# Kernel optimization log

Hardware: AMD Instinct MI355X
Metric: run time of the kernel (lower is better)

The kernel has to match this reference:

```python
import jax, jax.numpy as jnp
import numpy as np

DIM = 512
HEADS = 8
HEAD_DIM = DIM // HEADS
B, N = 2, 16 * 14 * 14  # input_size=(16,14,14) -> N=3136
SCALE = HEAD_DIM ** -0.5


def setup_inputs() -> dict:
    key = jax.random.key(0)
    kx, kq, kk, kv, kp = jax.random.split(key, 5)
    s = DIM ** -0.5  # keep pre-softmax logits reasonable
    return {
        "x": jax.random.normal(kx, (B, N, DIM), dtype=jnp.float32),
        "wq": jax.random.normal(kq, (DIM, DIM), dtype=jnp.float32) * s,
        "wk": jax.random.normal(kk, (DIM, DIM), dtype=jnp.float32) * s,
        "wv": jax.random.normal(kv, (DIM, DIM), dtype=jnp.float32) * s,
        "wproj": jax.random.normal(kp, (DIM, DIM), dtype=jnp.float32) * s,
    }


def reference(x, wq, wk, wv, wproj):
    Bs, Ns, C = x.shape
    # nn.Linear computes x @ W.T; split heads -> [B, H, N, hd]
    def heads(y):
        return y.reshape(Bs, Ns, HEADS, HEAD_DIM).transpose(0, 2, 1, 3)
    q = heads(x @ wq.T)
    k = heads(x @ wk.T)
    v = heads(x @ wv.T)
    attn = jnp.einsum("bhnd,bhmd->bhnm", q, k) * SCALE  # [B,H,N,N]
    attn = jax.nn.softmax(attn, axis=-1)
    out = jnp.einsum("bhnm,bhmd->bhnd", attn, v)
    out = out.transpose(0, 2, 1, 3).reshape(Bs, Ns, C)
    return out @ wproj.T
```

## Files before the change

kernel.cpp:

```cpp
#include <hip/hip_runtime.h>
#include <hip/hip_bf16.h>
#include <stdint.h>

#define SEQ   3136
#define NDIM  512
#define NBH   16
#define QROWS 50176
#define XE    3211264
#define WE    262144

typedef __bf16 bf16x8 __attribute__((ext_vector_type(8)));
typedef float  f32x4  __attribute__((ext_vector_type(4)));
typedef unsigned short u16;
typedef u16 u16x8 __attribute__((ext_vector_type(8)));
typedef u16 u16x4 __attribute__((ext_vector_type(4)));

__device__ __forceinline__ u16 bfr(float f) { return __builtin_bit_cast(u16, (__bf16)f); }
__device__ __forceinline__ int swzf(int row) { return (row & 3) | ((row >> 1) & 4); }
__device__ __forceinline__ f32x4 mfma16(bf16x8 a, bf16x8 b, f32x4 c) {
  return __builtin_amdgcn_mfma_f32_16x16x32_bf16(a, b, c, 0, 0, 0);
}
__device__ __forceinline__ bf16x8 lds_frag(const u16* base, int row, int logical) {
  return __builtin_bit_cast(bf16x8,
      *(const u16x8*)((const char*)base + row * 128 + (logical ^ (swzf(row) << 4))));
}
__device__ __forceinline__ bf16x8 ldb(const u16* smem, uint32_t boff) {
  return __builtin_bit_cast(bf16x8, *(const u16x8*)((const char*)smem + boff));
}
__device__ __forceinline__ void gload16(const void* g, void* l) {
  __builtin_amdgcn_global_load_lds((const __attribute__((address_space(1))) void*)g,
                                   (__attribute__((address_space(3))) void*)l, 16, 0, 0);
}

__device__ __forceinline__ void cvt8(const float* src, u16* dst) {
  const f32x4* p = (const f32x4*)src;
  f32x4 a = p[0], b = p[1];
  u16x8 o;
  o[0]=bfr(a[0]); o[1]=bfr(a[1]); o[2]=bfr(a[2]); o[3]=bfr(a[3]);
  o[4]=bfr(b[0]); o[5]=bfr(b[1]); o[6]=bfr(b[2]); o[7]=bfr(b[3]);
  *(u16x8*)dst = o;
}

extern "C" __global__ void cvt_all(const float* __restrict__ x, const float* __restrict__ wq,
                                   const float* __restrict__ wk, const float* __restrict__ wv,
                                   const float* __restrict__ wp,
                                   u16* __restrict__ xb, u16* __restrict__ wall) {
  size_t gid = (size_t)(blockIdx.x * 256 + threadIdx.x) * 8;
  if (gid < XE) {
    cvt8(x + gid, xb + gid);
  } else {
    size_t j = gid - XE;
    int which = (int)(j >> 18);
    const float* s = which == 0 ? wq : which == 1 ? wk : which == 2 ? wv : wp;
    cvt8(s + (j & (WE - 1)), wall + j);
  }
}

extern "C" __global__ __launch_bounds__(512)
void qkv_kernel(const u16* __restrict__ xb, const u16* __restrict__ wb,
                u16* __restrict__ Qg, u16* __restrict__ Kg, u16* __restrict__ Vtg)
{
  __shared__ __align__(16) u16 smem[4 * 8192];
  const int tid = threadIdx.x, lane = tid & 63, wid = tid >> 6;
  const int g = lane >> 4, lr = lane & 15;
  const int wr = wid >> 1, wc = wid & 1;
  const int m0 = blockIdx.x * 128;
  const int f0 = blockIdx.y * 128;
  const int which = f0 >> 9;
  const int f0w = f0 & 511;

  f32x4 acc[2][4] = {};

  auto stage = [&](int buf, int k0) {
#pragma unroll
    for (int c = 0; c < 2; ++c) {
      int chunk = c * 512 + tid;
      int row = chunk >> 3;
      int lc = (lane & 7) ^ swzf(row);
      gload16(xb + (size_t)(m0 + row) * NDIM + k0 + lc * 8,
              smem + buf * 8192 + (c * 512 + wid * 64) * 8);
      gload16(wb + (size_t)(f0 + row) * NDIM + k0 + lc * 8,
              smem + 16384 + buf * 8192 + (c * 512 + wid * 64) * 8);
    }
  };
  auto compute = [&](int buf) {
    const u16* A  = smem + buf * 8192;
    const u16* Bl = smem + 16384 + buf * 8192;
#pragma unroll
    for (int ks = 0; ks < 2; ++ks) {
      bf16x8 af[2], bg[4];
#pragma unroll
      for (int t = 0; t < 2; ++t) af[t] = lds_frag(A,  wr * 32 + t * 16 + lr, ks * 64 + g * 16);
#pragma unroll
      for (int t = 0; t < 4; ++t) bg[t] = lds_frag(Bl, wc * 64 + t * 16 + lr, ks * 64 + g * 16);
      __builtin_amdgcn_s_setprio(1);
#pragma unroll
      for (int tm = 0; tm < 2; ++tm)
#pragma unroll
        for (int tn = 0; tn < 4; ++tn)
          acc[tm][tn] = mfma16(af[tm], bg[tn], acc[tm][tn]);
      __builtin_amdgcn_s_setprio(0);
    }
  };

  stage(0, 0);
  __syncthreads();
  int buf = 0;
#pragma unroll 1
  for (int k = 0; k < 8; ++k) {
    if (k < 7) stage(buf ^ 1, (k + 1) * 64);
    compute(buf);
    __syncthreads();
    buf ^= 1;
  }

  const float qscale = 0.18033688f;
  if (which < 2) {
    u16* Dst = which == 0 ? Qg : Kg;
    float sc = which == 0 ? qscale : 1.0f;
#pragma unroll
    for (int tm = 0; tm < 2; ++tm)
#pragma unroll
      for (int tn = 0; tn < 4; ++tn)
#pragma unroll
        for (int r = 0; r < 4; ++r) {
          int m = m0 + wr * 32 + tm * 16 + 4 * g + r;
          int b = m >= SEQ; int n = m - b * SEQ;
          int fm = f0w + wc * 64 + tn * 16 + lr;
          int h = fm >> 6, d = fm & 63;
          Dst[(((size_t)(b * 8 + h)) * SEQ + n) * 64 + d] = bfr(acc[tm][tn][r] * sc);
        }
  } else {
    u16* T = smem;
#pragma unroll
    for (int tm = 0; tm < 2; ++tm)
#pragma unroll
      for (int tn = 0; tn < 4; ++tn) {
        int fl = wc * 64 + tn * 16 + lr;
        int t0r = wr * 32 + tm * 16 + 4 * g;
        u16x4 o;
        o[0]=bfr(acc[tm][tn][0]); o[1]=bfr(acc[tm][tn][1]);
        o[2]=bfr(acc[tm][tn][2]); o[3]=bfr(acc[tm][tn][3]);
        *(u16x4*)((char*)T + fl * 256 + ((t0r * 2) ^ ((fl & 7) << 4))) = o;
      }
    __syncthreads();
#pragma unroll
    for (int c = 0; c < 4; ++c) {
      int chunk = c * 512 + tid;
      int fl = chunk >> 4, tc = chunk & 15;
      int tb = tc * 16;
      u16x8 v = *(const u16x8*)((const char*)T + fl * 256 + (tb ^ ((fl & 7) << 4)));
      int fm = f0w + fl; int h = fm >> 6, d = fm & 63;
      int n0 = m0 + tc * 8;
      int b = n0 >= SEQ; n0 -= b * SEQ;
      *(u16x8*)(Vtg + (((size_t)(b * 8 + h)) * 64 + d) * SEQ + n0) = v;
    }
  }
}

extern "C" __global__ __launch_bounds__(256, 3)
void attn_kernel(const u16* __restrict__ Qg, const u16* __restrict__ Kg,
                 const u16* __restrict__ Vtg, float* __restrict__ Opart,
                 float* __restrict__ mlb)
{
  __shared__ __align__(16) u16 smem[16384];
  const int tid = threadIdx.x, lane = tid & 63, wid = tid >> 6;
  const int g = lane >> 4, lr = lane & 15;
  const int q0 = blockIdx.x * 128;
  const int bh = blockIdx.y;
  const int split = blockIdx.z;
  const size_t bhN = (size_t)bh * SEQ;

  bf16x8 qf[2][2];
#pragma unroll
  for (int qs = 0; qs < 2; ++qs) {
    int n = q0 + wid * 32 + qs * 16 + lr;
    n = n < SEQ ? n : SEQ - 1;
    const u16* qp = Qg + (bhN + n) * 64;
    qf[qs][0] = __builtin_bit_cast(bf16x8, *(const u16x8*)(qp + g * 8));
    qf[qs][1] = __builtin_bit_cast(bf16x8, *(const u16x8*)(qp + 32 + g * 8));
  }
  bf16x8 ones;
  {
    u16x8 ow;
#pragma unroll
    for (int j = 0; j < 8; ++j) ow[j] = 0x3F80;
    ones = __builtin_bit_cast(bf16x8, ow);
  }

  f32x4 om[2][4] = {};
  f32x4 lacc[2] = {};

  const int swk = ((lr & 3) | (((lr >> 2) & 1) << 2)) << 4;
  const uint32_t krow = (uint32_t)((lr >> 2) * 1024 + (lr & 3) * 128);
  const uint32_t kb0 = krow + ((g * 16) ^ swk);
  const uint32_t kb1 = krow + ((g * 16 + 64) ^ swk);
  const int swv = ((lr & 3) | ((lr >> 1) & 4)) << 4;
  const uint32_t vb0 = 8192 + lr * 128 + ((g * 16) ^ swv);
  const uint32_t vb1 = 8192 + lr * 128 + ((g * 16 + 64) ^ swv);

  uint32_t koff[2], voff[2];
#pragma unroll
  for (int c = 0; c < 2; ++c) {
    int row = wid * 16 + c * 8 + (lane >> 3);
    int lc = (lane & 7) ^ swzf(row);
    koff[c] = row * 64 + lc * 8;
    voff[c] = row * SEQ + lc * 8;
  }
  const int t0 = split * 25;
  const int nt = 25 - split;
  const u16* kp = Kg + (bhN + t0 * 64) * 64;
  const u16* vp = Vtg + (size_t)bh * (64 * (size_t)SEQ) + t0 * 64;

  auto stage_to = [&](int dstoff) {
#pragma unroll
    for (int c = 0; c < 2; ++c) {
      gload16(kp + koff[c], (char*)smem + dstoff + (wid * 2 + c) * 1024);
      gload16(vp + voff[c], (char*)smem + dstoff + 8192 + (wid * 2 + c) * 1024);
    }
  };

  int s = 0;
  stage_to(0); kp += 4096; vp += 64;
  __syncthreads();

  auto tile = [&](const int BOFF) {
    if (s + 1 < nt) { stage_to(BOFF ^ 16384); kp += 4096; vp += 64; }

    f32x4 st[2][4] = {};
#pragma unroll
    for (int ks = 0; ks < 2; ++ks) {
      const uint32_t kb = ks ? kb1 : kb0;
      bf16x8 kf[4];
#pragma unroll
      for (int kt = 0; kt < 4; ++kt)
        kf[kt] = ldb(smem, kb + BOFF + (kt & 1) * 4096 + (kt >> 1) * 512);
      __builtin_amdgcn_s_setprio(1);
#pragma unroll
      for (int kt = 0; kt < 4; ++kt) {
        st[0][kt] = mfma16(kf[kt], qf[0][ks], st[0][kt]);
        st[1][kt] = mfma16(kf[kt], qf[1][ks], st[1][kt]);
      }
      __builtin_amdgcn_s_setprio(0);
    }

    bf16x8 vf[4][2];
#pragma unroll
    for (int dt = 0; dt < 4; ++dt) {
      vf[dt][0] = ldb(smem, vb0 + BOFF + dt * 2048);
      vf[dt][1] = ldb(smem, vb1 + BOFF + dt * 2048);
    }

    bf16x8 pa[2][2];
#pragma unroll
    for (int qs = 0; qs < 2; ++qs)
#pragma unroll
      for (int kt = 0; kt < 4; ++kt)
#pragma unroll
        for (int r = 0; r < 4; ++r) {
          float e = exp2f(st[qs][kt][r]);
          pa[qs][kt & 1][(kt >> 1) * 4 + r] = (__bf16)e;
        }

    __builtin_amdgcn_s_setprio(1);
#pragma unroll
    for (int dt = 0; dt < 4; ++dt) {
      om[0][dt] = mfma16(vf[dt][0], pa[0][0], om[0][dt]);
      om[0][dt] = mfma16(vf[dt][1], pa[0][1], om[0][dt]);
      om[1][dt] = mfma16(vf[dt][0], pa[1][0], om[1][dt]);
      om[1][dt] = mfma16(vf[dt][1], pa[1][1], om[1][dt]);
    }
    __builtin_amdgcn_s_setprio(0);
    lacc[0] = mfma16(ones, pa[0][0], lacc[0]);
    lacc[0] = mfma16(ones, pa[0][1], lacc[0]);
    lacc[1] = mfma16(ones, pa[1][0], lacc[1]);
    lacc[1] = mfma16(ones, pa[1][1], lacc[1]);
    __syncthreads();
  };

  while (true) {
    tile(0);     if (++s == nt) break;
    tile(16384); if (++s == nt) break;
  }

#pragma unroll
  for (int qs = 0; qs < 2; ++qs) {
    int n = q0 + wid * 32 + qs * 16 + lr;
    if (n < SEQ) {
      float* Ob = Opart + ((size_t)(split * NBH + bh) * SEQ + n) * 64;
#pragma unroll
      for (int dt = 0; dt < 4; ++dt)
        *(f32x4*)(Ob + dt * 16 + 4 * g) = om[qs][dt];
      if (g == 0)
        mlb[(size_t)split * QROWS + bhN + n] = lacc[qs][0];
    }
  }
}

extern "C" __global__ void combine_kernel(const float* __restrict__ Opart,
                                          const float* __restrict__ mlb,
                                          u16* __restrict__ Og)
{
  const int tid = threadIdx.x;
  const int n = blockIdx.x * 32 + (tid >> 3);
  const int bh = blockIdx.y;
  const int dc = (tid & 7) * 8;
  const size_t R = (size_t)bh * SEQ + n;

  float inv = 1.0f / (mlb[R] + mlb[QROWS + R]);

  const float* p0 = Opart + R * 64 + dc;
  const float* p1 = Opart + (size_t)QROWS * 64 + R * 64 + dc;
  f32x4 o0a = *(const f32x4*)p0, o0b = *(const f32x4*)(p0 + 4);
  f32x4 o1a = *(const f32x4*)p1, o1b = *(const f32x4*)(p1 + 4);
  u16x8 o;
#pragma unroll
  for (int j = 0; j < 4; ++j) {
    o[j]     = bfr((o0a[j] + o1a[j]) * inv);
    o[4 + j] = bfr((o0b[j] + o1b[j]) * inv);
  }
  *(u16x8*)(Og + ((size_t)(bh >> 3) * SEQ + n) * NDIM + (bh & 7) * 64 + dc) = o;
}

extern "C" __global__ __launch_bounds__(256, 2)
void proj_kernel(const u16* __restrict__ Og, const u16* __restrict__ wpb,
                 float* __restrict__ out)
{
  __shared__ __align__(16) u16 smem[4 * 4096];
  const int tid = threadIdx.x, lane = tid & 63, wid = tid >> 6;
  const int g = lane >> 4, lr = lane & 15;
  const int m0 = blockIdx.x * 64;
  const int f0 = blockIdx.y * 64;

  f32x4 acc[4] = {};

  auto stage = [&](int buf, int k0) {
#pragma unroll
    for (int c = 0; c < 2; ++c) {
      int seg = wid * 2 + c;
      int row = seg * 8 + (lane >> 3);
      int lc = (lane & 7) ^ swzf(row);
      gload16(Og + (size_t)(m0 + row) * NDIM + k0 + lc * 8,
              smem + buf * 4096 + seg * 512);
      gload16(wpb + (size_t)(f0 + row) * NDIM + k0 + lc * 8,
              smem + 8192 + buf * 4096 + seg * 512);
    }
  };
  auto compute = [&](int buf) {
    const u16* A  = smem + buf * 4096;
    const u16* Bl = smem + 8192 + buf * 4096;
#pragma unroll
    for (int ks = 0; ks < 2; ++ks) {
      bf16x8 af = lds_frag(A, wid * 16 + lr, ks * 64 + g * 16);
#pragma unroll
      for (int t = 0; t < 4; ++t) {
        bf16x8 bg = lds_frag(Bl, t * 16 + lr, ks * 64 + g * 16);
        acc[t] = mfma16(af, bg, acc[t]);
      }
    }
  };

  stage(0, 0);
  __syncthreads();
  int buf = 0;
#pragma unroll 1
  for (int k = 0; k < 8; ++k) {
    if (k < 7) stage(buf ^ 1, (k + 1) * 64);
    compute(buf);
    __syncthreads();
    buf ^= 1;
  }

#pragma unroll
  for (int t = 0; t < 4; ++t)
#pragma unroll
    for (int r = 0; r < 4; ++r) {
      int m = m0 + wid * 16 + 4 * g + r;
      out[(size_t)m * NDIM + f0 + t * 16 + lr] = acc[t][r];
    }
}

extern "C" void kernel_launch(void* const* d_in, const int* in_sizes, int n_in,
                              void* d_out, int out_size, void* d_ws, size_t ws_size,
                              hipStream_t stream) {
  const float* x     = (const float*)d_in[0];
  const float* wq    = (const float*)d_in[1];
  const float* wk    = (const float*)d_in[2];
  const float* wv    = (const float*)d_in[3];
  const float* wproj = (const float*)d_in[4];
  float* out = (float*)d_out;

  const size_t E = (size_t)QROWS * 64;
  u16*   xb    = (u16*)d_ws;
  u16*   wall  = xb + XE;
  u16*   Qg    = wall + 4 * WE;
  u16*   Kg    = Qg + E;
  u16*   Vtg   = Kg + E;
  float* Opart = (float*)(Vtg + E);
  float* mlb   = Opart + 2 * E;
  u16*   Og    = xb;

  cvt_all       <<<dim3(2080),      256, 0, stream>>>(x, wq, wk, wv, wproj, xb, wall);
  qkv_kernel    <<<dim3(49, 12),    512, 0, stream>>>(xb, wall, Qg, Kg, Vtg);
  attn_kernel   <<<dim3(25, 16, 2), 256, 0, stream>>>(Qg, Kg, Vtg, Opart, mlb);
  combine_kernel<<<dim3(98, 16),    256, 0, stream>>>(Opart, mlb, Og);
  proj_kernel   <<<dim3(98, 8),     256, 0, stream>>>(Og, wall + 3 * WE, out);
}
```

Before: 175.5 us.

## Split attention KV range three ways and store normalized fp16 partials

Raises the KV split from two to three (17/16/16 tiles), giving 1200 attention blocks instead of 800 to improve CU occupancy and balance. Each split normalizes its output by its own row sum and stores fp16 partials instead of fp32, halving partial-output traffic. The combine kernel reads three partials and weights them by their row sums. The launch-bounds occupancy hint is dropped, and fp16 partials add rounding error.

```diff
diff --git a/kernel.cpp b/kernel.cpp
--- a/kernel.cpp
+++ b/kernel.cpp
@@ -8,14 +8,18 @@
 #define QROWS 50176
 #define XE    3211264
 #define WE    262144
+#define NSPLIT 3
 
 typedef __bf16 bf16x8 __attribute__((ext_vector_type(8)));
 typedef float  f32x4  __attribute__((ext_vector_type(4)));
 typedef unsigned short u16;
 typedef u16 u16x8 __attribute__((ext_vector_type(8)));
 typedef u16 u16x4 __attribute__((ext_vector_type(4)));
+typedef _Float16 f16;
 
 __device__ __forceinline__ u16 bfr(float f) { return __builtin_bit_cast(u16, (__bf16)f); }
+__device__ __forceinline__ u16 h16(float f) { return __builtin_bit_cast(u16, (f16)f); }
+__device__ __forceinline__ float h2f(u16 u) { return (float)__builtin_bit_cast(f16, u); }
 __device__ __forceinline__ int swzf(int row) { return (row & 3) | ((row >> 1) & 4); }
 __device__ __forceinline__ f32x4 mfma16(bf16x8 a, bf16x8 b, f32x4 c) {
   return __builtin_amdgcn_mfma_f32_16x16x32_bf16(a, b, c, 0, 0, 0);
@@ -158,9 +162,9 @@
   }
 }
 
-extern "C" __global__ __launch_bounds__(256, 3)
+extern "C" __global__ __launch_bounds__(256)
 void attn_kernel(const u16* __restrict__ Qg, const u16* __restrict__ Kg,
-                 const u16* __restrict__ Vtg, float* __restrict__ Opart,
+                 const u16* __restrict__ Vtg, u16* __restrict__ Opart,
                  float* __restrict__ mlb)
 {
   __shared__ __align__(16) u16 smem[16384];
@@ -199,6 +203,9 @@
   const uint32_t vb0 = 8192 + lr * 128 + ((g * 16) ^ swv);
   const uint32_t vb1 = 8192 + lr * 128 + ((g * 16 + 64) ^ swv);
 
+  const int t0 = split == 0 ? 0 : 16 * split + 1;
+  const int nt = split == 0 ? 17 : 16;
+
   uint32_t koff[2], voff[2];
 #pragma unroll
   for (int c = 0; c < 2; ++c) {
@@ -207,8 +214,6 @@
     koff[c] = row * 64 + lc * 8;
     voff[c] = row * SEQ + lc * 8;
   }
-  const int t0 = split * 25;
-  const int nt = 25 - split;
   const u16* kp = Kg + (bhN + t0 * 64) * 64;
   const u16* vp = Vtg + (size_t)bh * (64 * (size_t)SEQ) + t0 * 64;
 
@@ -287,17 +292,22 @@
   for (int qs = 0; qs < 2; ++qs) {
     int n = q0 + wid * 32 + qs * 16 + lr;
     if (n < SEQ) {
-      float* Ob = Opart + ((size_t)(split * NBH + bh) * SEQ + n) * 64;
-#pragma unroll
-      for (int dt = 0; dt < 4; ++dt)
-        *(f32x4*)(Ob + dt * 16 + 4 * g) = om[qs][dt];
+      float linv = 1.0f / lacc[qs][0];
+      u16* Ob = Opart + ((size_t)(split * NBH + bh) * SEQ + n) * 64;
+#pragma unroll
+      for (int dt = 0; dt < 4; ++dt) {
+        u16x4 o;
+        o[0] = h16(om[qs][dt][0] * linv); o[1] = h16(om[qs][dt][1] * linv);
+        o[2] = h16(om[qs][dt][2] * linv); o[3] = h16(om[qs][dt][3] * linv);
+        *(u16x4*)(Ob + dt * 16 + 4 * g) = o;
+      }
       if (g == 0)
         mlb[(size_t)split * QROWS + bhN + n] = lacc[qs][0];
     }
   }
 }
 
-extern "C" __global__ void combine_kernel(const float* __restrict__ Opart,
+extern "C" __global__ void combine_kernel(const u16* __restrict__ Opart,
                                           const float* __restrict__ mlb,
                                           u16* __restrict__ Og)
 {
@@ -307,18 +317,17 @@
   const int dc = (tid & 7) * 8;
   const size_t R = (size_t)bh * SEQ + n;
 
-  float inv = 1.0f / (mlb[R] + mlb[QROWS + R]);
-
-  const float* p0 = Opart + R * 64 + dc;
-  const float* p1 = Opart + (size_t)QROWS * 64 + R * 64 + dc;
-  f32x4 o0a = *(const f32x4*)p0, o0b = *(const f32x4*)(p0 + 4);
-  f32x4 o1a = *(const f32x4*)p1, o1b = *(const f32x4*)(p1 + 4);
+  float l0 = mlb[R], l1 = mlb[QROWS + R], l2 = mlb[2 * QROWS + R];
+  float inv = 1.0f / (l0 + l1 + l2);
+  float w0 = l0 * inv, w1 = l1 * inv, w2 = l2 * inv;
+
+  u16x8 v0 = *(const u16x8*)(Opart + (0 * (size_t)QROWS + R) * 64 + dc);
+  u16x8 v1 = *(const u16x8*)(Opart + (1 * (size_t)QROWS + R) * 64 + dc);
+  u16x8 v2 = *(const u16x8*)(Opart + (2 * (size_t)QROWS + R) * 64 + dc);
   u16x8 o;
 #pragma unroll
-  for (int j = 0; j < 4; ++j) {
-    o[j]     = bfr((o0a[j] + o1a[j]) * inv);
-    o[4 + j] = bfr((o0b[j] + o1b[j]) * inv);
-  }
+  for (int j = 0; j < 8; ++j)
+    o[j] = bfr(w0 * h2f(v0[j]) + w1 * h2f(v1[j]) + w2 * h2f(v2[j]));
   *(u16x8*)(Og + ((size_t)(bh >> 3) * SEQ + n) * NDIM + (bh & 7) * 64 + dc) = o;
 }
 
@@ -396,13 +405,13 @@
   u16*   Qg    = wall + 4 * WE;
   u16*   Kg    = Qg + E;
   u16*   Vtg   = Kg + E;
-  float* Opart = (float*)(Vtg + E);
-  float* mlb   = Opart + 2 * E;
+  u16*   Opart = Vtg + E;
+  float* mlb   = (float*)(Opart + NSPLIT * E);
   u16*   Og    = xb;
 
-  cvt_all       <<<dim3(2080),      256, 0, stream>>>(x, wq, wk, wv, wproj, xb, wall);
-  qkv_kernel    <<<dim3(49, 12),    512, 0, stream>>>(xb, wall, Qg, Kg, Vtg);
-  attn_kernel   <<<dim3(25, 16, 2), 256, 0, stream>>>(Qg, Kg, Vtg, Opart, mlb);
-  combine_kernel<<<dim3(98, 16),    256, 0, stream>>>(Opart, mlb, Og);
-  proj_kernel   <<<dim3(98, 8),     256, 0, stream>>>(Og, wall + 3 * WE, out);
-}
+  cvt_all       <<<dim3(2080),           256, 0, stream>>>(x, wq, wk, wv, wproj, xb, wall);
+  qkv_kernel    <<<dim3(49, 12),         512, 0, stream>>>(xb, wall, Qg, Kg, Vtg);
+  attn_kernel   <<<dim3(25, 16, NSPLIT), 256, 0, stream>>>(Qg, Kg, Vtg, Opart, mlb);
+  combine_kernel<<<dim3(98, 16),         256, 0, stream>>>(Opart, mlb, Og);
+  proj_kernel   <<<dim3(98, 8),          256, 0, stream>>>(Og, wall + 3 * WE, out);
+}
```

Result: no change. 175.1 us (-0.3%).
